# Kernel tuning notes

Measured on AMD Instinct MI355X. Metric: run time of the kernel, lower is better.

## Reference

```python
import jax, jax.numpy as jnp
import numpy as np

N_USERS = 100_000
N_ITEMS = 50_000
E = 2_000_000
B = 100_000
DU, DI, H, L = 256, 128, 64, 2
EPS = 1e-5  # BatchNorm eps


def setup_inputs() -> dict:
    key = jax.random.key(0)
    ks = jax.random.split(key, 32)
    f32 = jnp.float32
    inp = {
        "user_features": jax.random.normal(ks[0], (N_USERS, DU), f32),
        "item_features": jax.random.normal(ks[1], (N_ITEMS, DI), f32),
        "edge_index": jnp.stack([
            jax.random.randint(ks[2], (E,), 0, N_USERS),
            jax.random.randint(ks[3], (E,), 0, N_ITEMS),
        ]).astype(jnp.int32),
        "edge_label_index": jnp.stack([
            jax.random.randint(ks[4], (B,), 0, N_USERS),
            jax.random.randint(ks[5], (B,), 0, N_ITEMS),
        ]).astype(jnp.int32),
        # projections (stored as [in, out])
        "user_proj_W": jax.random.normal(ks[6], (DU, H), f32) * 0.05,
        "user_proj_b": jax.random.normal(ks[7], (H,), f32) * 0.05,
        "item_proj_W": jax.random.normal(ks[8], (DI, H), f32) * 0.05,
        "item_proj_b": jax.random.normal(ks[9], (H,), f32) * 0.05,
        # SAGEConv weights stacked over layers: lin_l (aggr neighbors, with bias), lin_r (self, no bias)
        "u_lin_l_W": jax.random.normal(ks[10], (L, H, H), f32) * 0.1,
        "u_lin_l_b": jax.random.normal(ks[11], (L, H), f32) * 0.05,
        "u_lin_r_W": jax.random.normal(ks[12], (L, H, H), f32) * 0.1,
        "i_lin_l_W": jax.random.normal(ks[13], (L, H, H), f32) * 0.1,
        "i_lin_l_b": jax.random.normal(ks[14], (L, H), f32) * 0.05,
        "i_lin_r_W": jax.random.normal(ks[15], (L, H, H), f32) * 0.1,
        # BatchNorm (eval mode: affine + running stats)
        "u_bn_gamma": 1.0 + jax.random.normal(ks[16], (L, H), f32) * 0.05,
        "u_bn_beta": jax.random.normal(ks[17], (L, H), f32) * 0.05,
        "u_bn_mean": jax.random.normal(ks[18], (L, H), f32) * 0.05,
        "u_bn_var": jax.random.uniform(ks[19], (L, H), f32, 0.5, 1.5),
        "i_bn_gamma": 1.0 + jax.random.normal(ks[20], (L, H), f32) * 0.05,
        "i_bn_beta": jax.random.normal(ks[21], (L, H), f32) * 0.05,
        "i_bn_mean": jax.random.normal(ks[22], (L, H), f32) * 0.05,
        "i_bn_var": jax.random.uniform(ks[23], (L, H), f32, 0.5, 1.5),
        # final MLP head
        "fc1_W": jax.random.normal(ks[24], (2 * H, H), f32) * 0.1,
        "fc1_b": jax.random.normal(ks[25], (H,), f32) * 0.05,
        "fc2_W": jax.random.normal(ks[26], (H, 4), f32) * 0.1,
        "fc2_b": jax.random.normal(ks[27], (4,), f32) * 0.05,
    }
    return inp


def _bn(x, g, b, m, v):
    return (x - m) * (g * jax.lax.rsqrt(v + EPS)) + b


def _forward(user_features, item_features, edge_index, edge_label_index,
             user_proj_W, user_proj_b, item_proj_W, item_proj_b,
             u_lin_l_W, u_lin_l_b, u_lin_r_W,
             i_lin_l_W, i_lin_l_b, i_lin_r_W,
             u_bn_gamma, u_bn_beta, u_bn_mean, u_bn_var,
             i_bn_gamma, i_bn_beta, i_bn_mean, i_bn_var,
             fc1_W, fc1_b, fc2_W, fc2_b):
    src, dst = edge_index[0], edge_index[1]  # user idx, item idx
    ux = user_features @ user_proj_W + user_proj_b  # [Nu, H]
    ix = item_features @ item_proj_W + item_proj_b  # [Ni, H]
    # in-degree of items (for mean aggregation), clamp for isolated nodes
    deg_i = jnp.clip(jax.ops.segment_sum(jnp.ones((E,), ux.dtype), dst, N_ITEMS), 1.0)[:, None]
    for l in range(L):
        # user conv: aggr='max' over item neighbors (edge_index flipped)
        agg_u = jax.ops.segment_max(ix[dst], src, num_segments=N_USERS)
        agg_u = jnp.where(jnp.isfinite(agg_u), agg_u, 0.0)  # empty segments -> 0 (PyG behavior)
        u_new = agg_u @ u_lin_l_W[l] + u_lin_l_b[l] + ux @ u_lin_r_W[l]
        u_new = jax.nn.relu(_bn(u_new, u_bn_gamma[l], u_bn_beta[l], u_bn_mean[l], u_bn_var[l]))
        # item conv: aggr='mean' over user neighbors
        agg_i = jax.ops.segment_sum(ux[src], dst, num_segments=N_ITEMS) / deg_i
        i_new = agg_i @ i_lin_l_W[l] + i_lin_l_b[l] + ix @ i_lin_r_W[l]
        i_new = jax.nn.relu(_bn(i_new, i_bn_gamma[l], i_bn_beta[l], i_bn_mean[l], i_bn_var[l]))
        ux, ix = u_new, i_new
    uh = ux[edge_label_index[0]]  # [B, H]
    ih = ix[edge_label_index[1]]  # [B, H]
    x = jnp.concatenate([uh, ih], axis=1)  # [B, 2H]
    return jax.nn.relu(x @ fc1_W + fc1_b) @ fc2_W + fc2_b  # [B, 4]


def reference(user_features, item_features, edge_index, edge_label_index,
              user_proj_W, user_proj_b, item_proj_W, item_proj_b,
              u_lin_l_W, u_lin_l_b, u_lin_r_W,
              i_lin_l_W, i_lin_l_b, i_lin_r_W,
              u_bn_gamma, u_bn_beta, u_bn_mean, u_bn_var,
              i_bn_gamma, i_bn_beta, i_bn_mean, i_bn_var,
              fc1_W, fc1_b, fc2_W, fc2_b):
    return _forward(user_features, item_features, edge_index, edge_label_index,
                    user_proj_W, user_proj_b, item_proj_W, item_proj_b,
                    u_lin_l_W, u_lin_l_b, u_lin_r_W,
                    i_lin_l_W, i_lin_l_b, i_lin_r_W,
                    u_bn_gamma, u_bn_beta, u_bn_mean, u_bn_var,
                    i_bn_gamma, i_bn_beta, i_bn_mean, i_bn_var,
                    fc1_W, fc1_b, fc2_W, fc2_b)
```

## Files before the change

kernel.cpp:

```cpp
#include <hip/hip_runtime.h>
#include <math.h>

#define N_USERS 100000
#define N_ITEMS 50000
#define NE      2000000
#define NB      100000
#define H       64
#define BN_EPS  1e-5f
#define P_PART  8
#define U_LOC   (N_USERS / P_PART)
#define I_LOC   (N_ITEMS / P_PART)
#define HSLOTS  (U_LOC + I_LOC)
#define S_SLICES 50
#define NBLK_CSR (P_PART * S_SLICES)
#define E_SLICE  (NE / S_SLICES)
#define Q_SLICE  (E_SLICE / 4)
#define SCAN_CHUNK 2048
#define T_CSR   512

typedef __attribute__((ext_vector_type(8))) short bf16x8;
typedef __attribute__((ext_vector_type(4))) float f32x4;
typedef __attribute__((ext_vector_type(4))) int   i32x4;

static __device__ __forceinline__ int rfl(int x) { return __builtin_amdgcn_readfirstlane(x); }

static __device__ __forceinline__ unsigned short f2bf(float f) {
  union { float f; unsigned u; } v; v.f = f;
  const unsigned r = v.u + 0x7fffu + ((v.u >> 16) & 1u);
  return (unsigned short)(r >> 16);
}
static __device__ __forceinline__ float bf2f(unsigned short h) {
  union { unsigned u; float f; } v; v.u = (unsigned)h << 16;
  return v.f;
}
static __device__ __forceinline__ float bfu_lo(unsigned x) {
  union { unsigned u; float f; } v; v.u = x << 16;
  return v.f;
}
static __device__ __forceinline__ float bfu_hi(unsigned x) {
  union { unsigned u; float f; } v; v.u = x & 0xffff0000u;
  return v.f;
}

__global__ __launch_bounds__(256) void pack_kernel(
    const float* __restrict__ upW, const float* __restrict__ ipW,
    const float* __restrict__ ulW, const float* __restrict__ urW,
    const float* __restrict__ ilW, const float* __restrict__ irW,
    const float* __restrict__ f1W, unsigned short* __restrict__ dst) {
  const int b = blockIdx.x;
  const int ct = threadIdx.x >> 6, lane = threadIdx.x & 63;
  const float* src;
  int krow0;
  if (b < 8)       { src = upW; krow0 = b * 32; }
  else if (b < 12) { src = ipW; krow0 = (b - 8) * 32; }
  else if (b < 28) {
    const int idx = b - 12, t = idx >> 2, ks = idx & 3;
    const int layer = t & 1;
    const float* Wl = (t < 2) ? ulW : ilW;
    const float* Wr = (t < 2) ? urW : irW;
    src = ((ks < 2) ? Wl : Wr) + layer * 4096;
    krow0 = ((ks < 2) ? ks : ks - 2) * 32;
  } else { src = f1W; krow0 = (b - 28) * 32; }
  unsigned short* out = dst + (size_t)b * 2048 + ((size_t)ct * 64 + lane) * 8;
  const int col = ct * 16 + (lane & 15);
  const int kr = krow0 + (lane >> 4) * 8;
#pragma unroll
  for (int j = 0; j < 8; j++) out[j] = f2bf(src[(kr + j) * 64 + col]);
}

template<int K>
__global__ __launch_bounds__(256) void proj_mfma(
    const float* __restrict__ X, const unsigned short* __restrict__ Wf,
    const float* __restrict__ bias, unsigned short* __restrict__ Y, int nrows) {
  const int lane = threadIdx.x & 63;
  const int wave = rfl((int)(threadIdx.x >> 6));
  const int r0 = (blockIdx.x * 4 + wave) * 16;
  if (r0 >= nrows) return;
  const int arow = r0 + (lane & 15);
  const int ar = arow < nrows ? arow : nrows - 1;
  const int k0 = (lane >> 4) * 8;
  f32x4 acc[4] = {};
#pragma unroll
  for (int ks = 0; ks < K / 32; ks++) {
    const float* xp = X + (size_t)ar * K + ks * 32 + k0;
    const float4 xa = *reinterpret_cast<const float4*>(xp);
    const float4 xb = *reinterpret_cast<const float4*>(xp + 4);
    bf16x8 af;
    af[0] = f2bf(xa.x); af[1] = f2bf(xa.y); af[2] = f2bf(xa.z); af[3] = f2bf(xa.w);
    af[4] = f2bf(xb.x); af[5] = f2bf(xb.y); af[6] = f2bf(xb.z); af[7] = f2bf(xb.w);
#pragma unroll
    for (int ct = 0; ct < 4; ct++) {
      const bf16x8 bfr = *reinterpret_cast<const bf16x8*>(
          Wf + ((size_t)(ks * 4 + ct) * 64 + lane) * 8);
      acc[ct] = __builtin_amdgcn_mfma_f32_16x16x32_bf16(af, bfr, acc[ct], 0, 0, 0);
    }
  }
  const int orow0 = r0 + (lane >> 4) * 4;
#pragma unroll
  for (int ct = 0; ct < 4; ct++) {
    const int col = ct * 16 + (lane & 15);
    const float bv = bias[col];
#pragma unroll
    for (int i = 0; i < 4; i++) {
      const int r = orow0 + i;
      if (r < nrows) Y[(size_t)r * 64 + col] = f2bf(acc[ct][i] + bv);
    }
  }
}

__global__ __launch_bounds__(256) void conv_mfma(
    const unsigned short* __restrict__ AGG, const unsigned short* __restrict__ XS,
    const unsigned short* __restrict__ Wf, const float* __restrict__ bl,
    const float* __restrict__ gm, const float* __restrict__ bt,
    const float* __restrict__ mu, const float* __restrict__ vr,
    unsigned short* __restrict__ Y, int nrows) {
  const int lane = threadIdx.x & 63;
  const int wave = rfl((int)(threadIdx.x >> 6));
  const int r0 = (blockIdx.x * 4 + wave) * 16;
  if (r0 >= nrows) return;
  const int arow = r0 + (lane & 15);
  const int ar = arow < nrows ? arow : nrows - 1;
  const int k0 = (lane >> 4) * 8;
  f32x4 acc[4] = {};
#pragma unroll
  for (int ks = 0; ks < 4; ks++) {
    const unsigned short* ap =
        (ks < 2 ? AGG : XS) + (size_t)ar * 64 + (ks & 1) * 32 + k0;
    const bf16x8 af = *reinterpret_cast<const bf16x8*>(ap);
#pragma unroll
    for (int ct = 0; ct < 4; ct++) {
      const bf16x8 bfr = *reinterpret_cast<const bf16x8*>(
          Wf + ((size_t)(ks * 4 + ct) * 64 + lane) * 8);
      acc[ct] = __builtin_amdgcn_mfma_f32_16x16x32_bf16(af, bfr, acc[ct], 0, 0, 0);
    }
  }
  const int orow0 = r0 + (lane >> 4) * 4;
#pragma unroll
  for (int ct = 0; ct < 4; ct++) {
    const int col = ct * 16 + (lane & 15);
    const float s = gm[col] * rsqrtf(vr[col] + BN_EPS);
    const float C = (bl[col] - mu[col]) * s + bt[col];
#pragma unroll
    for (int i = 0; i < 4; i++) {
      const int r = orow0 + i;
      if (r < nrows)
        Y[(size_t)r * 64 + col] = f2bf(fmaxf(fmaf(acc[ct][i], s, C), 0.f));
    }
  }
}

__global__ __launch_bounds__(T_CSR) void hist2_kernel(
    const int* __restrict__ src, const int* __restrict__ dst,
    unsigned short* __restrict__ PH) {
  __shared__ int h[HSLOTS];
  const int p = blockIdx.x & (P_PART - 1);
  const int s = blockIdx.x >> 3;
  for (int i = threadIdx.x; i < HSLOTS; i += T_CSR) h[i] = 0;
  __syncthreads();
  const int uLo = p * U_LOC, iLo = p * I_LOC;
  const int e0 = s * E_SLICE;
  const i32x4* s4 = reinterpret_cast<const i32x4*>(src + e0);
  const i32x4* d4 = reinterpret_cast<const i32x4*>(dst + e0);
  for (int i = threadIdx.x; i < Q_SLICE; i += T_CSR) {
    const i32x4 us = s4[i];
    const i32x4 ds = d4[i];
#pragma unroll
    for (int q = 0; q < 4; q++) {
      const int ul = us[q] - uLo;
      if ((unsigned)ul < (unsigned)U_LOC) atomicAdd(&h[ul], 1);
      const int il = ds[q] - iLo;
      if ((unsigned)il < (unsigned)I_LOC) atomicAdd(&h[U_LOC + il], 1);
    }
  }
  __syncthreads();
  unsigned short* out = PH + (size_t)blockIdx.x * HSLOTS;
  for (int i = threadIdx.x; i < HSLOTS; i += T_CSR)
    __builtin_nontemporal_store((unsigned short)h[i], &out[i]);
}

__global__ __launch_bounds__(256) void combine_kernel(
    unsigned short* __restrict__ PH, int* __restrict__ cntU,
    int* __restrict__ cntI) {
  const int g = blockIdx.x * 256 + threadIdx.x;
  if (g >= P_PART * HSLOTS) return;
  const int x = g / HSLOTS;
  const int n = g - x * HSLOTS;
  unsigned short* p = PH + (size_t)x * HSLOTS + n;
  int run = 0;
#pragma unroll 2
  for (int s = 0; s < S_SLICES; s++) {
    unsigned short* q = p + (size_t)s * (P_PART * HSLOTS);
    const int v = (int)__builtin_nontemporal_load(q);
    __builtin_nontemporal_store((unsigned short)run, q);
    run += v;
  }
  if (n < U_LOC) cntU[x * U_LOC + n] = run;
  else           cntI[x * I_LOC + (n - U_LOC)] = run;
}

__global__ __launch_bounds__(256) void scan1_kernel(
    const int* __restrict__ cnt, int* __restrict__ row,
    int* __restrict__ bsum, int n) {
  __shared__ int wtot[4];
  const int tid = threadIdx.x;
  const int lane = tid & 63, wv = tid >> 6;
  const int i0 = blockIdx.x * SCAN_CHUNK + tid * 8;
  int sacc[8];
  int run = 0;
#pragma unroll
  for (int k = 0; k < 8; k++) {
    const int v = (i0 + k < n) ? cnt[i0 + k] : 0;
    run += v;
    sacc[k] = run;
  }
  int x = run;
#pragma unroll
  for (int off = 1; off < 64; off <<= 1) {
    const int y = __shfl_up(x, off);
    if (lane >= off) x += y;
  }
  if (lane == 63) wtot[wv] = x;
  __syncthreads();
  int woff = 0;
#pragma unroll
  for (int k = 0; k < 4; k++) woff += (k < wv) ? wtot[k] : 0;
  const int excl = (x - run) + woff;
#pragma unroll
  for (int k = 0; k < 8; k++)
    if (i0 + k < n) row[i0 + k + 1] = excl + sacc[k];
  if (tid == 255) bsum[blockIdx.x] = excl + run;
}

__global__ __launch_bounds__(256) void scan3_kernel(
    const int* __restrict__ bsum, int* __restrict__ row, int n) {
  __shared__ int off_s;
  const int b = blockIdx.x;
  const int tid = threadIdx.x;
  if (tid < 64) {
    int v = (tid < b) ? bsum[tid] : 0;
#pragma unroll
    for (int off = 32; off; off >>= 1) v += __shfl_xor(v, off);
    if (tid == 0) off_s = v;
  }
  __syncthreads();
  const int off = off_s;
  if (b == 0) {
    if (tid == 0) row[0] = 0;
    return;
  }
  const int i0 = b * SCAN_CHUNK + tid * 8;
#pragma unroll
  for (int k = 0; k < 8; k++)
    if (i0 + k < n) row[i0 + k + 1] += off;
}

__global__ __launch_bounds__(T_CSR) void scatter2_kernel(
    const int* __restrict__ src, const int* __restrict__ dst,
    const unsigned short* __restrict__ PH, const int* __restrict__ rowU,
    const int* __restrict__ rowI, int* __restrict__ adjU,
    int* __restrict__ adjI) {
  __shared__ int pos[HSLOTS];
  const int p = blockIdx.x & (P_PART - 1);
  const int s = blockIdx.x >> 3;
  const int uLo = p * U_LOC, iLo = p * I_LOC;
  const unsigned short* pre = PH + (size_t)blockIdx.x * HSLOTS;
  for (int i = threadIdx.x; i < U_LOC; i += T_CSR)
    pos[i] = rowU[uLo + i] + (int)__builtin_nontemporal_load(&pre[i]);
  for (int i = threadIdx.x; i < I_LOC; i += T_CSR)
    pos[U_LOC + i] = rowI[iLo + i] + (int)__builtin_nontemporal_load(&pre[U_LOC + i]);
  __syncthreads();
  const int e0 = s * E_SLICE;
  const i32x4* s4 = reinterpret_cast<const i32x4*>(src + e0);
  const i32x4* d4 = reinterpret_cast<const i32x4*>(dst + e0);
  for (int i = threadIdx.x; i < Q_SLICE; i += T_CSR) {
    const i32x4 us = s4[i];
    const i32x4 ds = d4[i];
#pragma unroll
    for (int q = 0; q < 4; q++) {
      const int u = us[q], it = ds[q];
      const int ul = u - uLo, il = it - iLo;
      if ((unsigned)ul < (unsigned)U_LOC) {
        const int pp = atomicAdd(&pos[ul], 1);
        adjU[pp] = it;
      }
      if ((unsigned)il < (unsigned)I_LOC) {
        const int pp = atomicAdd(&pos[U_LOC + il], 1);
        adjI[pp] = u;
      }
    }
  }
}

__global__ __launch_bounds__(256) void agg_max_kernel(
    const unsigned short* __restrict__ feat, const int* __restrict__ rowptr,
    const int* __restrict__ adj, unsigned short* __restrict__ out, int nseg) {
  const int lane = threadIdx.x & 63;
  const int wid  = rfl((int)(threadIdx.x >> 6));
  const int g    = lane >> 4;
  const int c4   = (lane & 15) * 4;
  for (int s = blockIdx.x * 4 + wid; s < nseg; s += gridDim.x * 4) {
    const int beg = rowptr[s], end = rowptr[s + 1];
    float m0 = -INFINITY, m1 = -INFINITY, m2 = -INFINITY, m3 = -INFINITY;
    float n0 = -INFINITY, n1 = -INFINITY, n2 = -INFINITY, n3 = -INFINITY;
    int j = beg;
    for (; j + 8 <= end; j += 8) {
      const int ia = adj[j + g];
      const int ib = adj[j + 4 + g];
      const uint2 va = *reinterpret_cast<const uint2*>(feat + (size_t)ia * H + c4);
      const uint2 vb = *reinterpret_cast<const uint2*>(feat + (size_t)ib * H + c4);
      m0 = fmaxf(m0, bfu_lo(va.x)); m1 = fmaxf(m1, bfu_hi(va.x));
      m2 = fmaxf(m2, bfu_lo(va.y)); m3 = fmaxf(m3, bfu_hi(va.y));
      n0 = fmaxf(n0, bfu_lo(vb.x)); n1 = fmaxf(n1, bfu_hi(vb.x));
      n2 = fmaxf(n2, bfu_lo(vb.y)); n3 = fmaxf(n3, bfu_hi(vb.y));
    }
    for (; j < end; j += 4) {
      if (j + g < end) {
        const int ia = adj[j + g];
        const uint2 va = *reinterpret_cast<const uint2*>(feat + (size_t)ia * H + c4);
        m0 = fmaxf(m0, bfu_lo(va.x)); m1 = fmaxf(m1, bfu_hi(va.x));
        m2 = fmaxf(m2, bfu_lo(va.y)); m3 = fmaxf(m3, bfu_hi(va.y));
      }
    }
    m0 = fmaxf(m0, n0); m1 = fmaxf(m1, n1);
    m2 = fmaxf(m2, n2); m3 = fmaxf(m3, n3);
    m0 = fmaxf(m0, __shfl_xor(m0, 16)); m0 = fmaxf(m0, __shfl_xor(m0, 32));
    m1 = fmaxf(m1, __shfl_xor(m1, 16)); m1 = fmaxf(m1, __shfl_xor(m1, 32));
    m2 = fmaxf(m2, __shfl_xor(m2, 16)); m2 = fmaxf(m2, __shfl_xor(m2, 32));
    m3 = fmaxf(m3, __shfl_xor(m3, 16)); m3 = fmaxf(m3, __shfl_xor(m3, 32));
    if (lane < 16) {
      uint2 o;
      if (end > beg) {
        o.x = (unsigned)f2bf(m0) | ((unsigned)f2bf(m1) << 16);
        o.y = (unsigned)f2bf(m2) | ((unsigned)f2bf(m3) << 16);
      } else {
        o.x = 0; o.y = 0;
      }
      *reinterpret_cast<uint2*>(out + (size_t)s * H + c4) = o;
    }
  }
}

__global__ __launch_bounds__(256) void agg_mean_kernel(
    const unsigned short* __restrict__ feat, const int* __restrict__ rowptr,
    const int* __restrict__ adj, unsigned short* __restrict__ out, int nseg) {
  const int lane = threadIdx.x & 63;
  const int wid  = rfl((int)(threadIdx.x >> 6));
  const int g    = lane >> 4;
  const int c4   = (lane & 15) * 4;
  for (int s = blockIdx.x * 4 + wid; s < nseg; s += gridDim.x * 4) {
    const int beg = rowptr[s], end = rowptr[s + 1];
    float a0 = 0.f, a1 = 0.f, a2 = 0.f, a3 = 0.f;
    float b0 = 0.f, b1 = 0.f, b2 = 0.f, b3 = 0.f;
    int j = beg;
    for (; j + 8 <= end; j += 8) {
      const int ia = adj[j + g];
      const int ib = adj[j + 4 + g];
      const uint2 va = *reinterpret_cast<const uint2*>(feat + (size_t)ia * H + c4);
      const uint2 vb = *reinterpret_cast<const uint2*>(feat + (size_t)ib * H + c4);
      a0 += bfu_lo(va.x); a1 += bfu_hi(va.x);
      a2 += bfu_lo(va.y); a3 += bfu_hi(va.y);
      b0 += bfu_lo(vb.x); b1 += bfu_hi(vb.x);
      b2 += bfu_lo(vb.y); b3 += bfu_hi(vb.y);
    }
    for (; j < end; j += 4) {
      if (j + g < end) {
        const int ia = adj[j + g];
        const uint2 va = *reinterpret_cast<const uint2*>(feat + (size_t)ia * H + c4);
        a0 += bfu_lo(va.x); a1 += bfu_hi(va.x);
        a2 += bfu_lo(va.y); a3 += bfu_hi(va.y);
      }
    }
    a0 += b0; a1 += b1; a2 += b2; a3 += b3;
    a0 += __shfl_xor(a0, 16); a0 += __shfl_xor(a0, 32);
    a1 += __shfl_xor(a1, 16); a1 += __shfl_xor(a1, 32);
    a2 += __shfl_xor(a2, 16); a2 += __shfl_xor(a2, 32);
    a3 += __shfl_xor(a3, 16); a3 += __shfl_xor(a3, 32);
    if (lane < 16) {
      const float inv = 1.f / (float)((end - beg) > 1 ? (end - beg) : 1);
      uint2 o;
      o.x = (unsigned)f2bf(a0 * inv) | ((unsigned)f2bf(a1 * inv) << 16);
      o.y = (unsigned)f2bf(a2 * inv) | ((unsigned)f2bf(a3 * inv) << 16);
      *reinterpret_cast<uint2*>(out + (size_t)s * H + c4) = o;
    }
  }
}

__global__ __launch_bounds__(256) void head_mfma(
    const unsigned short* __restrict__ ux, const unsigned short* __restrict__ ix,
    const int* __restrict__ eliU, const int* __restrict__ eliI,
    const unsigned short* __restrict__ W1f, const float* __restrict__ b1,
    const float* __restrict__ W2, const float* __restrict__ b2,
    float* __restrict__ out) {
  const int lane = threadIdx.x & 63;
  const int wave = rfl((int)(threadIdx.x >> 6));
  const int r0 = (blockIdx.x * 4 + wave) * 16;
  if (r0 >= NB) return;
  const int rr = r0 + (lane & 15);
  const int rc = rr < NB ? rr : NB - 1;
  const int idxU = eliU[rc], idxI = eliI[rc];
  const int k0 = (lane >> 4) * 8;
  f32x4 acc[4] = {};
#pragma unroll
  for (int ks = 0; ks < 4; ks++) {
    const unsigned short* ap = (ks < 2)
        ? ux + (size_t)idxU * 64 + (ks & 1) * 32 + k0
        : ix + (size_t)idxI * 64 + (ks & 1) * 32 + k0;
    const bf16x8 af = *reinterpret_cast<const bf16x8*>(ap);
#pragma unroll
    for (int ct = 0; ct < 4; ct++) {
      const bf16x8 bfr = *reinterpret_cast<const bf16x8*>(
          W1f + ((size_t)(ks * 4 + ct) * 64 + lane) * 8);
      acc[ct] = __builtin_amdgcn_mfma_f32_16x16x32_bf16(af, bfr, acc[ct], 0, 0, 0);
    }
  }
  float p[4][4];
#pragma unroll
  for (int i = 0; i < 4; i++)
#pragma unroll
    for (int o = 0; o < 4; o++) p[i][o] = 0.f;
#pragma unroll
  for (int ct = 0; ct < 4; ct++) {
    const int col = ct * 16 + (lane & 15);
    const float bb = b1[col];
    const float wa = W2[col * 4 + 0], wb = W2[col * 4 + 1];
    const float wc = W2[col * 4 + 2], wd = W2[col * 4 + 3];
#pragma unroll
    for (int i = 0; i < 4; i++) {
      const float h = fmaxf(acc[ct][i] + bb, 0.f);
      p[i][0] = fmaf(h, wa, p[i][0]);
      p[i][1] = fmaf(h, wb, p[i][1]);
      p[i][2] = fmaf(h, wc, p[i][2]);
      p[i][3] = fmaf(h, wd, p[i][3]);
    }
  }
#pragma unroll
  for (int off = 1; off < 16; off <<= 1) {
#pragma unroll
    for (int i = 0; i < 4; i++) {
      p[i][0] += __shfl_xor(p[i][0], off);
      p[i][1] += __shfl_xor(p[i][1], off);
      p[i][2] += __shfl_xor(p[i][2], off);
      p[i][3] += __shfl_xor(p[i][3], off);
    }
  }
  if ((lane & 15) == 0) {
    const int row0 = r0 + (lane >> 4) * 4;
#pragma unroll
    for (int i = 0; i < 4; i++) {
      const int r = row0 + i;
      if (r < NB) {
        float4 o4 = { p[i][0] + b2[0], p[i][1] + b2[1],
                      p[i][2] + b2[2], p[i][3] + b2[3] };
        *reinterpret_cast<float4*>(out + (size_t)r * 4) = o4;
      }
    }
  }
}

extern "C" void kernel_launch(void* const* d_in, const int* in_sizes, int n_in,
                              void* d_out, int out_size, void* d_ws, size_t ws_size,
                              hipStream_t stream) {
  const float* userF = (const float*)d_in[0];
  const float* itemF = (const float*)d_in[1];
  const int*   src   = (const int*)d_in[2];
  const int*   dst   = src + NE;
  const int*   eliU  = (const int*)d_in[3];
  const int*   eliI  = eliU + NB;
  const float* upW = (const float*)d_in[4],  *upb = (const float*)d_in[5];
  const float* ipW = (const float*)d_in[6],  *ipb = (const float*)d_in[7];
  const float* ulW = (const float*)d_in[8],  *ulb = (const float*)d_in[9];
  const float* urW = (const float*)d_in[10];
  const float* ilW = (const float*)d_in[11], *ilb = (const float*)d_in[12];
  const float* irW = (const float*)d_in[13];
  const float* ug  = (const float*)d_in[14], *ube = (const float*)d_in[15];
  const float* um  = (const float*)d_in[16], *uv  = (const float*)d_in[17];
  const float* ig  = (const float*)d_in[18], *ibe = (const float*)d_in[19];
  const float* im  = (const float*)d_in[20], *iv  = (const float*)d_in[21];
  const float* f1W = (const float*)d_in[22], *f1b = (const float*)d_in[23];
  const float* f2W = (const float*)d_in[24], *f2b = (const float*)d_in[25];
  float* outp = (float*)d_out;

  char* p = (char*)d_ws;
  auto alloc = [&](size_t bytes) {
    char* r = p;
    p += (bytes + 255) & ~(size_t)255;
    return r;
  };
  unsigned short* ux0 = (unsigned short*)alloc((size_t)N_USERS * H * 2);
  unsigned short* ix0 = (unsigned short*)alloc((size_t)N_ITEMS * H * 2);
  char* grp = alloc((size_t)38400 * 1024);
  unsigned short* agU = (unsigned short*)grp;
  unsigned short* agI = agU + (size_t)N_USERS * H;
  unsigned short* ux1 = agI + (size_t)N_ITEMS * H;
  unsigned short* ix1 = ux1 + (size_t)N_USERS * H;
  unsigned short* PH = (unsigned short*)grp;
  int*   rowU = (int*)alloc((size_t)(N_USERS + 1) * 4);
  int*   rowI = (int*)alloc((size_t)(N_ITEMS + 1) * 4);
  int*   cntU = (int*)alloc((size_t)N_USERS * 4);
  int*   cntI = (int*)alloc((size_t)N_ITEMS * 4);
  int*   adjU = (int*)alloc((size_t)NE * 4);
  int*   adjI = (int*)alloc((size_t)NE * 4);
  int*   bsumU = (int*)alloc(64 * 4);
  int*   bsumI = (int*)alloc(64 * 4);
  unsigned short* wpack = (unsigned short*)alloc((size_t)32 * 2048 * 2);

  const int G = 2048, T = 256;
  const int SBU = (N_USERS + SCAN_CHUNK - 1) / SCAN_CHUNK;
  const int SBI = (N_ITEMS + SCAN_CHUNK - 1) / SCAN_CHUNK;
  pack_kernel<<<32, T, 0, stream>>>(upW, ipW, ulW, urW, ilW, irW, f1W, wpack);
  proj_mfma<256><<<(N_USERS + 63) / 64, T, 0, stream>>>(userF, wpack, upb, ux0, N_USERS);
  proj_mfma<128><<<(N_ITEMS + 63) / 64, T, 0, stream>>>(itemF, wpack + 8 * 2048, ipb, ix0, N_ITEMS);
  hist2_kernel<<<NBLK_CSR, T_CSR, 0, stream>>>(src, dst, PH);
  combine_kernel<<<(P_PART * HSLOTS + 255) / 256, T, 0, stream>>>(PH, cntU, cntI);
  scan1_kernel<<<SBU, T, 0, stream>>>(cntU, rowU, bsumU, N_USERS);
  scan1_kernel<<<SBI, T, 0, stream>>>(cntI, rowI, bsumI, N_ITEMS);
  scan3_kernel<<<SBU, T, 0, stream>>>(bsumU, rowU, N_USERS);
  scan3_kernel<<<SBI, T, 0, stream>>>(bsumI, rowI, N_ITEMS);
  scatter2_kernel<<<NBLK_CSR, T_CSR, 0, stream>>>(src, dst, PH, rowU, rowI, adjU, adjI);

  const unsigned short* uin = ux0;
  const unsigned short* iin = ix0;
  unsigned short* uout = ux1;
  unsigned short* iout = ix1;
  const int GU = (N_USERS + 63) / 64, GI = (N_ITEMS + 63) / 64;
  for (int l = 0; l < 2; l++) {
    unsigned short* cwU = wpack + (12 + 4 * (0 + l)) * 2048;
    unsigned short* cwI = wpack + (12 + 4 * (2 + l)) * 2048;
    agg_max_kernel<<<G, T, 0, stream>>>(iin, rowU, adjU, agU, N_USERS);
    conv_mfma<<<GU, T, 0, stream>>>(agU, uin, cwU, ulb + l * 64,
                                    ug + l * 64, ube + l * 64,
                                    um + l * 64, uv + l * 64, uout, N_USERS);
    agg_mean_kernel<<<G, T, 0, stream>>>(uin, rowI, adjI, agI, N_ITEMS);
    conv_mfma<<<GI, T, 0, stream>>>(agI, iin, cwI, ilb + l * 64,
                                    ig + l * 64, ibe + l * 64,
                                    im + l * 64, iv + l * 64, iout, N_ITEMS);
    const unsigned short* t;
    t = uin; uin = uout; uout = (unsigned short*)t;
    t = iin; iin = iout; iout = (unsigned short*)t;
  }
  head_mfma<<<(NB / 16 + 3) / 4, T, 0, stream>>>(uin, iin, eliU, eliI,
                                                 wpack + 28 * 2048, f1b, f2W, f2b, outp);
}
```

Before: 377.7 us.

## Fuse histogram and feature projection kernels into one heterogeneous launch

Merges the two projection MFMA kernels and the edge histogram kernel into one launch whose blocks branch on block index to do either histogram work or projection work. Projection blocks now use 512 threads (8 waves of 16 rows each) so they share the launch config with the histogram. The goal is to overlap the memory-bound projection with the atomic-heavy LDS histogram and to drop two launch gaps. In exchange, every block reserves the large static LDS histogram array even when it only does projection, which may cut occupancy for the projection blocks.

```diff
diff --git a/kernel.cpp b/kernel.cpp
--- a/kernel.cpp
+++ b/kernel.cpp
@@ -17,6 +17,8 @@
 #define Q_SLICE  (E_SLICE / 4)
 #define SCAN_CHUNK 2048
 #define T_CSR   512
+#define GU_BLK  ((N_USERS + 127) / 128)
+#define GI_BLK  ((N_ITEMS + 127) / 128)
 
 typedef __attribute__((ext_vector_type(8))) short bf16x8;
 typedef __attribute__((ext_vector_type(4))) float f32x4;
@@ -69,12 +71,13 @@
 }
 
 template<int K>
-__global__ __launch_bounds__(256) void proj_mfma(
+static __device__ __forceinline__ void proj_body(
     const float* __restrict__ X, const unsigned short* __restrict__ Wf,
-    const float* __restrict__ bias, unsigned short* __restrict__ Y, int nrows) {
+    const float* __restrict__ bias, unsigned short* __restrict__ Y,
+    int nrows, int bp) {
   const int lane = threadIdx.x & 63;
   const int wave = rfl((int)(threadIdx.x >> 6));
-  const int r0 = (blockIdx.x * 4 + wave) * 16;
+  const int r0 = (bp * 8 + wave) * 16;
   if (r0 >= nrows) return;
   const int arow = r0 + (lane & 15);
   const int ar = arow < nrows ? arow : nrows - 1;
@@ -105,6 +108,47 @@
       const int r = orow0 + i;
       if (r < nrows) Y[(size_t)r * 64 + col] = f2bf(acc[ct][i] + bv);
     }
+  }
+}
+
+__global__ __launch_bounds__(T_CSR) void fused_hist_proj(
+    const int* __restrict__ src, const int* __restrict__ dst,
+    unsigned short* __restrict__ PH,
+    const float* __restrict__ userF, const float* __restrict__ itemF,
+    const unsigned short* __restrict__ wpack,
+    const float* __restrict__ upb, const float* __restrict__ ipb,
+    unsigned short* __restrict__ ux0, unsigned short* __restrict__ ix0) {
+  __shared__ int h[HSLOTS];
+  const int b = blockIdx.x;
+  if (b < NBLK_CSR) {
+    const int p = b & (P_PART - 1);
+    const int s = b >> 3;
+    for (int i = threadIdx.x; i < HSLOTS; i += T_CSR) h[i] = 0;
+    __syncthreads();
+    const int uLo = p * U_LOC, iLo = p * I_LOC;
+    const int e0 = s * E_SLICE;
+    const i32x4* s4 = reinterpret_cast<const i32x4*>(src + e0);
+    const i32x4* d4 = reinterpret_cast<const i32x4*>(dst + e0);
+    for (int i = threadIdx.x; i < Q_SLICE; i += T_CSR) {
+      const i32x4 us = s4[i];
+      const i32x4 ds = d4[i];
+#pragma unroll
+      for (int q = 0; q < 4; q++) {
+        const int ul = us[q] - uLo;
+        if ((unsigned)ul < (unsigned)U_LOC) atomicAdd(&h[ul], 1);
+        const int il = ds[q] - iLo;
+        if ((unsigned)il < (unsigned)I_LOC) atomicAdd(&h[U_LOC + il], 1);
+      }
+    }
+    __syncthreads();
+    unsigned short* out = PH + (size_t)b * HSLOTS;
+    for (int i = threadIdx.x; i < HSLOTS; i += T_CSR)
+      __builtin_nontemporal_store((unsigned short)h[i], &out[i]);
+  } else if (b < NBLK_CSR + GU_BLK) {
+    proj_body<256>(userF, wpack, upb, ux0, N_USERS, b - NBLK_CSR);
+  } else {
+    proj_body<128>(itemF, wpack + 8 * 2048, ipb, ix0, N_ITEMS,
+                   b - NBLK_CSR - GU_BLK);
   }
 }
 
@@ -147,35 +191,6 @@
         Y[(size_t)r * 64 + col] = f2bf(fmaxf(fmaf(acc[ct][i], s, C), 0.f));
     }
   }
-}
-
-__global__ __launch_bounds__(T_CSR) void hist2_kernel(
-    const int* __restrict__ src, const int* __restrict__ dst,
-    unsigned short* __restrict__ PH) {
-  __shared__ int h[HSLOTS];
-  const int p = blockIdx.x & (P_PART - 1);
-  const int s = blockIdx.x >> 3;
-  for (int i = threadIdx.x; i < HSLOTS; i += T_CSR) h[i] = 0;
-  __syncthreads();
-  const int uLo = p * U_LOC, iLo = p * I_LOC;
-  const int e0 = s * E_SLICE;
-  const i32x4* s4 = reinterpret_cast<const i32x4*>(src + e0);
-  const i32x4* d4 = reinterpret_cast<const i32x4*>(dst + e0);
-  for (int i = threadIdx.x; i < Q_SLICE; i += T_CSR) {
-    const i32x4 us = s4[i];
-    const i32x4 ds = d4[i];
-#pragma unroll
-    for (int q = 0; q < 4; q++) {
-      const int ul = us[q] - uLo;
-      if ((unsigned)ul < (unsigned)U_LOC) atomicAdd(&h[ul], 1);
-      const int il = ds[q] - iLo;
-      if ((unsigned)il < (unsigned)I_LOC) atomicAdd(&h[U_LOC + il], 1);
-    }
-  }
-  __syncthreads();
-  unsigned short* out = PH + (size_t)blockIdx.x * HSLOTS;
-  for (int i = threadIdx.x; i < HSLOTS; i += T_CSR)
-    __builtin_nontemporal_store((unsigned short)h[i], &out[i]);
 }
 
 __global__ __launch_bounds__(256) void combine_kernel(
@@ -508,9 +523,8 @@
   const int SBU = (N_USERS + SCAN_CHUNK - 1) / SCAN_CHUNK;
   const int SBI = (N_ITEMS + SCAN_CHUNK - 1) / SCAN_CHUNK;
   pack_kernel<<<32, T, 0, stream>>>(upW, ipW, ulW, urW, ilW, irW, f1W, wpack);
-  proj_mfma<256><<<(N_USERS + 63) / 64, T, 0, stream>>>(userF, wpack, upb, ux0, N_USERS);
-  proj_mfma<128><<<(N_ITEMS + 63) / 64, T, 0, stream>>>(itemF, wpack + 8 * 2048, ipb, ix0, N_ITEMS);
-  hist2_kernel<<<NBLK_CSR, T_CSR, 0, stream>>>(src, dst, PH);
+  fused_hist_proj<<<NBLK_CSR + GU_BLK + GI_BLK, T_CSR, 0, stream>>>(
+      src, dst, PH, userF, itemF, wpack, upb, ipb, ux0, ix0);
   combine_kernel<<<(P_PART * HSLOTS + 255) / 256, T, 0, stream>>>(PH, cntU, cntI);
   scan1_kernel<<<SBU, T, 0, stream>>>(cntU, rowU, bsumU, N_USERS);
   scan1_kernel<<<SBI, T, 0, stream>>>(cntI, rowI, bsumI, N_ITEMS);
```

Result: faster. 368.3 us, median of 3 (-2.5%).
